# Kernel tuning notes

Hardware: AMD Instinct MI355X
Metric: run time of the kernel (lower is better)

## Reference

```python
import jax, jax.numpy as jnp
import numpy as np
from jax.ops import segment_sum, segment_max

N_NODES, N_EDGES, N_GRAPHS = 50000, 800000, 128
IN_C, HID, HEADS, CLIN = 64, 64, 4, 32


def gat_layer(x, W, a_s, a_d, b, src, dst, n):
    # GAT-style attention conv with concatenated heads (PyG GATConv math).
    H, C = a_s.shape
    h = (x @ W).reshape(-1, H, C)                      # [N,H,C]
    es = jnp.einsum('nhc,hc->nh', h, a_s)
    ed = jnp.einsum('nhc,hc->nh', h, a_d)
    e = jax.nn.leaky_relu(es[src] + ed[dst], 0.2)      # [E,H]
    m = segment_max(e, dst, num_segments=n)            # stable softmax over incoming edges
    e = jnp.exp(e - m[dst])
    denom = segment_sum(e, dst, num_segments=n)
    alpha = e / jnp.where(denom[dst] > 0, denom[dst], 1.0)
    out = segment_sum(h[src] * alpha[:, :, None], dst, num_segments=n)  # [N,H,C]
    return out.reshape(-1, H * C) + b


def label_prop(x, src, dst, n, num_layers=2, alpha=0.5):
    # PyG LabelPropagation: sym-normalized diffusion, residual mix, clamp to [0,1].
    deg = segment_sum(jnp.ones((src.shape[0],), x.dtype), dst, num_segments=n)
    dis = jnp.where(deg > 0, 1.0 / jnp.sqrt(jnp.maximum(deg, 1.0)), 0.0)
    norm = (dis[src] * dis[dst])[:, None]
    res = (1.0 - alpha) * x
    out = x
    for _ in range(num_layers):
        out = alpha * segment_sum(out[src] * norm, dst, num_segments=n) + res
        out = jnp.clip(out, 0.0, 1.0)
    return out


def mean_pool(x, batch, n_graphs):
    cnt = segment_sum(jnp.ones((x.shape[0],), x.dtype), batch, num_segments=n_graphs)
    s = segment_sum(x, batch, num_segments=n_graphs)
    return s / jnp.maximum(cnt, 1.0)[:, None]


def setup_inputs() -> dict:
    key = jax.random.key(0)
    ks = iter(jax.random.split(key, 32))
    def p(shape, fan_in):
        return jax.random.normal(next(ks), shape, jnp.float32) / np.sqrt(fan_in)
    d = {}
    d['x'] = jax.random.normal(next(ks), (N_NODES, IN_C), jnp.float32)
    d['edge_index'] = jax.random.randint(next(ks), (2, N_EDGES), 0, N_NODES)
    d['batch'] = jnp.sort(jax.random.randint(next(ks), (N_NODES,), 0, N_GRAPHS))
    d['clinical_data'] = jax.random.normal(next(ks), (N_GRAPHS, CLIN), jnp.float32)
    HC = HEADS * HID
    d['W1'] = p((IN_C, HC), IN_C); d['a1s'] = p((HEADS, HID), HID); d['a1d'] = p((HEADS, HID), HID); d['b1'] = jnp.zeros((HC,), jnp.float32)
    d['W2'] = p((HC, HC), HC); d['a2s'] = p((HEADS, HID), HID); d['a2d'] = p((HEADS, HID), HID); d['b2'] = jnp.zeros((HC,), jnp.float32)
    jk = IN_C + 2 * HC  # 576
    d['pp_w1'] = p((jk, 256), jk); d['pp_b1'] = jnp.zeros((256,), jnp.float32)
    d['pp_w2'] = p((256, 128), 256); d['pp_b2'] = jnp.zeros((128,), jnp.float32)
    d['cl_w1'] = p((CLIN, 64), CLIN); d['cl_b1'] = jnp.zeros((64,), jnp.float32)
    d['cl_w2'] = p((64, 32), 64); d['cl_b2'] = jnp.zeros((32,), jnp.float32)
    d['h_w1'] = p((160, 64), 160); d['h_b1'] = jnp.zeros((64,), jnp.float32)
    d['h_w2'] = p((64, 32), 64); d['h_b2'] = jnp.zeros((32,), jnp.float32)
    d['h_w3'] = p((32, 2), 32); d['h_b3'] = jnp.zeros((2,), jnp.float32)
    return d


def reference(x, edge_index, batch, clinical_data,
              W1, a1s, a1d, b1, W2, a2s, a2d, b2,
              pp_w1, pp_b1, pp_w2, pp_b2,
              cl_w1, cl_b1, cl_w2, cl_b2,
              h_w1, h_b1, h_w2, h_b2, h_w3, h_b3):
    src, dst = edge_index[0], edge_index[1]
    n = x.shape[0]
    h0 = x
    h1 = jax.nn.relu(gat_layer(h0, W1, a1s, a1d, b1, src, dst, n))
    h1 = label_prop(h1, src, dst, n)
    h2 = jax.nn.relu(gat_layer(h1, W2, a2s, a2d, b2, src, dst, n))
    h2 = label_prop(h2, src, dst, n)
    combined = jnp.concatenate([h0, h1, h2], axis=-1)           # [N, 576]
    g = mean_pool(combined, batch, N_GRAPHS)                    # [G, 576]
    v_graph = jax.nn.relu(g @ pp_w1 + pp_b1) @ pp_w2 + pp_b2    # [G, 128] (dropout = eval/no-op)
    v_clin = jax.nn.relu(clinical_data @ cl_w1 + cl_b1) @ cl_w2 + cl_b2  # [G, 32]
    z = jnp.concatenate([v_graph, v_clin], axis=-1)             # [G, 160]
    z = jax.nn.relu(z @ h_w1 + h_b1)
    z = jax.nn.relu(z @ h_w2 + h_b2)
    return z @ h_w3 + h_b3                                      # [G, 2]
```

## Files before the change

### kernel.cpp

```cpp
#include <hip/hip_runtime.h>

#define N_NODES 50000
#define N_EDGES 800000
#define N_GRAPHS 128
#define JK 576
#define CAP 192
#define NSB ((N_NODES + 255) / 256)

typedef __attribute__((ext_vector_type(8))) short bf16x8;
typedef __attribute__((ext_vector_type(4))) float f32x4;

__device__ __forceinline__ unsigned f2_to_bf2(float a, float b) {
    unsigned ua = __float_as_uint(a), ub = __float_as_uint(b);
    ua = (ua + 0x7fffu + ((ua >> 16) & 1u)) >> 16;
    ub = (ub + 0x7fffu + ((ub >> 16) & 1u)) >> 16;
    return ua | (ub << 16);
}
__device__ __forceinline__ uint2 f4_to_bf4(float4 v) {
    return make_uint2(f2_to_bf2(v.x, v.y), f2_to_bf2(v.z, v.w));
}
__device__ __forceinline__ float4 bf4_to_f4(uint2 u) {
    float4 r;
    r.x = __uint_as_float(u.x << 16);
    r.y = __uint_as_float(u.x & 0xffff0000u);
    r.z = __uint_as_float(u.y << 16);
    r.w = __uint_as_float(u.y & 0xffff0000u);
    return r;
}

template<int BN, int KK>
__global__ __launch_bounds__(256)
void mfma_gemm(const unsigned short* __restrict__ Abf, int lda,
               const unsigned short* __restrict__ BT,
               unsigned* __restrict__ Cbf, int ldc,
               int M, const float* __restrict__ bias, int relu,
               int a_off, int b_off, int c_off) {
    __shared__ unsigned short As[64][32];
    __shared__ unsigned short Bs[BN][32];
    const int t = threadIdx.x;
    const int wav = t >> 6, lane = t & 63;
    const int quad = lane >> 4, l15 = lane & 15;
    const int m0 = blockIdx.x * 64;
    const int head = blockIdx.y;
    Abf += (size_t)head * a_off;
    BT  += (size_t)head * b_off;
    const float* bptr = bias ? bias + (size_t)head * c_off : nullptr;
    unsigned* cbf = Cbf + (((size_t)head * c_off) >> 1);

    f32x4 acc[BN / 16];
#pragma unroll
    for (int i = 0; i < BN / 16; i++) acc[i] = (f32x4){0.f, 0.f, 0.f, 0.f};

    const int arow = t >> 2, aseg = t & 3;
    for (int k0 = 0; k0 < KK; k0 += 32) {
        uint4 av = make_uint4(0, 0, 0, 0);
        int gm = m0 + arow;
        if (gm < M) av = *(const uint4*)&Abf[(size_t)gm * lda + k0 + aseg * 8];
        uint4 bv[BN == 256 ? 4 : 1];
        if (BN == 256) {
            const unsigned short* srcb = &BT[(size_t)t * KK + k0];
#pragma unroll
            for (int j = 0; j < 4; j++) bv[j] = *(const uint4*)&srcb[j * 8];
        } else {
            bv[0] = *(const uint4*)&BT[(size_t)arow * KK + k0 + aseg * 8];
        }
        __syncthreads();
        *(uint4*)&As[arow][aseg * 8] = av;
        if (BN == 256) {
#pragma unroll
            for (int j = 0; j < 4; j++) *(uint4*)&Bs[t][j * 8] = bv[j];
        } else {
            *(uint4*)&Bs[arow][aseg * 8] = bv[0];
        }
        __syncthreads();
        bf16x8 afrag = *(const bf16x8*)&As[wav * 16 + l15][quad * 8];
#pragma unroll
        for (int nt = 0; nt < BN / 16; nt++) {
            bf16x8 bfrag = *(const bf16x8*)&Bs[nt * 16 + l15][quad * 8];
            acc[nt] = __builtin_amdgcn_mfma_f32_16x16x32_bf16(afrag, bfrag, acc[nt], 0, 0, 0);
        }
    }
    int rbase = m0 + wav * 16 + quad * 4;
#pragma unroll
    for (int nt = 0; nt < BN / 16; nt++) {
        int col = nt * 16 + l15;
        float bb = bptr ? bptr[col] : 0.f;
#pragma unroll
        for (int r = 0; r < 4; r++) {
            int row = rbase + r;
            float v = acc[nt][r] + bb;
            if (relu) v = fmaxf(v, 0.f);
            float vp = __shfl_xor(v, 1);
            if (row < M && !(l15 & 1))
                cbf[((size_t)row * ldc + col) >> 1] = f2_to_bf2(v, vp);
        }
    }
}

__global__ void deg_kernel(const int* __restrict__ dst, int* __restrict__ deg,
                           const int* __restrict__ batch, int* __restrict__ gstart) {
    int t = blockIdx.x * blockDim.x + threadIdx.x;
    if (t < N_EDGES) {
        atomicAdd(&deg[dst[t]], 1);
    } else if (t < N_EDGES + N_NODES) {
        int n = t - N_EDGES;
        int b = batch[n];
        int prev = (n == 0) ? -1 : batch[n - 1];
        for (int g = prev + 1; g <= b; g++) gstart[g] = n;
        if (n == N_NODES - 1)
            for (int g = b + 1; g <= N_GRAPHS; g++) gstart[g] = N_NODES;
    }
}

#define S1 50000
#define S2 50256
#define S3 51280
#define S4 67664
#define S5 133200
#define S6 1733200
#define S7 (S6 + 131072)
__global__ void prep_misc(const int* __restrict__ deg, float* __restrict__ dis,
                          const float* __restrict__ W1, const float* __restrict__ a1s,
                          const float* __restrict__ a1d, float* __restrict__ wes1,
                          float* __restrict__ wed1,
                          const float* __restrict__ W2, const float* __restrict__ a2s,
                          const float* __restrict__ a2d, float* __restrict__ wes2,
                          float* __restrict__ wed2,
                          unsigned short* __restrict__ W1T, unsigned short* __restrict__ W2T,
                          const float* __restrict__ x, unsigned* __restrict__ xbf,
                          const int* __restrict__ gstart, float* __restrict__ psum) {
    int i = blockIdx.x * blockDim.x + threadIdx.x;
    if (i >= S7) return;
    if (i >= S6) {
        int t2 = i - S6;
        int g = t2 >> 10, rem = t2 & 1023;
        int q = rem >> 8, tid = rem & 255;
        int cp = tid & 63, np = tid >> 6;
        int n0 = gstart[g], n1 = gstart[g + 1];
        int len = n1 - n0;
        int ns = n0 + (len * q) / 4, ne = n0 + (len * (q + 1)) / 4;
        float s = 0.f;
        for (int n = ns + np; n < ne; n += 4) s += x[(size_t)n * 64 + cp];
        atomicAdd(&psum[g * JK + cp], s);
    } else if (i >= S5) {
        int j = i - S5;
        float2 v = *(const float2*)&x[(size_t)j * 2];
        xbf[j] = f2_to_bf2(v.x, v.y);
    } else if (i >= S4) {
        int t2 = i - S4;
        int n = t2 >> 8, c = t2 & 255;
        unsigned u = __float_as_uint(W2[(size_t)c * 256 + n]);
        u = (u + 0x7fffu + ((u >> 16) & 1u)) >> 16;
        W2T[t2] = (unsigned short)u;
    } else if (i >= S3) {
        int t2 = i - S3;
        int n = t2 >> 6, c = t2 & 63;
        unsigned u = __float_as_uint(W1[(size_t)c * 256 + n]);
        u = (u + 0x7fffu + ((u >> 16) & 1u)) >> 16;
        W1T[t2] = (unsigned short)u;
    } else if (i >= S2) {
        int t2 = i - S2;
        int c = t2 >> 2, h = t2 & 3;
        float se = 0.f, sd = 0.f;
        for (int j = 0; j < 64; j++) {
            float w = W2[(size_t)c * 256 + h * 64 + j];
            se += w * a2s[h * 64 + j];
            sd += w * a2d[h * 64 + j];
        }
        wes2[c * 4 + h] = se;
        wed2[c * 4 + h] = sd;
    } else if (i >= S1) {
        int t2 = i - S1;
        int c = t2 >> 2, h = t2 & 3;
        float se = 0.f, sd = 0.f;
        for (int j = 0; j < 64; j++) {
            float w = W1[(size_t)c * 256 + h * 64 + j];
            se += w * a1s[h * 64 + j];
            sd += w * a1d[h * 64 + j];
        }
        wes1[c * 4 + h] = se;
        wed1[c * 4 + h] = sd;
    } else {
        int d = deg[i];
        dis[i] = d > 0 ? rsqrtf((float)d) : 0.f;
    }
}
__global__ __launch_bounds__(256) void scan_bsum(const int* __restrict__ deg,
                                                 int* __restrict__ bsum) {
    __shared__ int sd[256];
    int n = blockIdx.x * 256 + threadIdx.x;
    sd[threadIdx.x] = (n < N_NODES) ? deg[n] : 0;
    __syncthreads();
    for (int o = 128; o > 0; o >>= 1) {
        if (threadIdx.x < o) sd[threadIdx.x] += sd[threadIdx.x + o];
        __syncthreads();
    }
    if (threadIdx.x == 0) bsum[blockIdx.x] = sd[0];
}
__global__ __launch_bounds__(256) void scan_bpre(const int* __restrict__ bsum,
                                                 int* __restrict__ bpre,
                                                 int* __restrict__ off_last) {
    __shared__ int sd[256];
    int t = threadIdx.x;
    int v = (t < NSB) ? bsum[t] : 0;
    sd[t] = v;
    __syncthreads();
    for (int o = 1; o < 256; o <<= 1) {
        int u = (t >= o) ? sd[t - o] : 0;
        __syncthreads();
        sd[t] += u;
        __syncthreads();
    }
    if (t < NSB) bpre[t] = sd[t] - v;
    if (t == 255) *off_last = sd[255];
}
__global__ __launch_bounds__(256) void scan_off(const int* __restrict__ deg,
                                                const int* __restrict__ bpre,
                                                int* __restrict__ off) {
    __shared__ int sd[256];
    int n = blockIdx.x * 256 + threadIdx.x;
    int t = threadIdx.x;
    int v = (n < N_NODES) ? deg[n] : 0;
    sd[t] = v;
    __syncthreads();
    for (int o = 1; o < 256; o <<= 1) {
        int u = (t >= o) ? sd[t - o] : 0;
        __syncthreads();
        sd[t] += u;
        __syncthreads();
    }
    if (n < N_NODES) off[n] = bpre[blockIdx.x] + sd[t] - v;
}
__global__ void csr_fill(const int* __restrict__ src, const int* __restrict__ dst,
                         const int* __restrict__ off, int* __restrict__ cursor,
                         int* __restrict__ csr_src) {
    int e = blockIdx.x * blockDim.x + threadIdx.x;
    if (e >= N_EDGES) return;
    int s = src[e], d = dst[e];
    int pos = off[d] + atomicAdd(&cursor[d], 1);
    csr_src[pos] = s;
}

__global__ void esed_x(const float* __restrict__ X, const float* __restrict__ wes,
                       const float* __restrict__ wed, float* __restrict__ es,
                       float* __restrict__ ed) {
    int gid = blockIdx.x * blockDim.x + threadIdx.x;
    int n = gid >> 6, lane = threadIdx.x & 63;
    if (n >= N_NODES) return;
    float xv = X[(size_t)n * 64 + lane];
    float4 a = *(const float4*)&wes[lane * 4];
    float4 b = *(const float4*)&wed[lane * 4];
    float4 ps = make_float4(xv * a.x, xv * a.y, xv * a.z, xv * a.w);
    float4 pd = make_float4(xv * b.x, xv * b.y, xv * b.z, xv * b.w);
#pragma unroll
    for (int o = 1; o < 64; o <<= 1) {
        ps.x += __shfl_xor(ps.x, o); ps.y += __shfl_xor(ps.y, o);
        ps.z += __shfl_xor(ps.z, o); ps.w += __shfl_xor(ps.w, o);
        pd.x += __shfl_xor(pd.x, o); pd.y += __shfl_xor(pd.y, o);
        pd.z += __shfl_xor(pd.z, o); pd.w += __shfl_xor(pd.w, o);
    }
    if (lane == 0) {
        *(float4*)&es[n * 4] = ps;
        *(float4*)&ed[n * 4] = pd;
    }
}

__global__ __launch_bounds__(256)
void gat1_fused(const int* __restrict__ off, const int* __restrict__ csr_src,
                const float* __restrict__ es, const float* __restrict__ ed,
                const unsigned* __restrict__ xbf, unsigned* __restrict__ aggx_bf,
                float* __restrict__ alpha_fb) {
    __shared__ float elds[4][CAP * 4];
    __shared__ int   sidx[4][CAP];
    int wav = threadIdx.x >> 6, lane = threadIdx.x & 63;
    int n = blockIdx.x * 4 + wav;
    bool active = n < N_NODES;
    int p0 = 0, p1 = 0;
    float4 ed4 = make_float4(0.f, 0.f, 0.f, 0.f);
    if (active) { p0 = off[n]; p1 = off[n + 1]; ed4 = *(const float4*)&ed[n * 4]; }
    float4 sum = make_float4(0.f, 0.f, 0.f, 0.f);
    for (int p = p0 + lane; p < p1; p += 64) {
        int s = csr_src[p];
        float4 e4 = *(const float4*)&es[s * 4];
        e4.x += ed4.x; e4.y += ed4.y; e4.z += ed4.z; e4.w += ed4.w;
        e4.x = e4.x > 0.f ? e4.x : 0.2f * e4.x;
        e4.y = e4.y > 0.f ? e4.y : 0.2f * e4.y;
        e4.z = e4.z > 0.f ? e4.z : 0.2f * e4.z;
        e4.w = e4.w > 0.f ? e4.w : 0.2f * e4.w;
        e4.x = __expf(e4.x); e4.y = __expf(e4.y); e4.z = __expf(e4.z); e4.w = __expf(e4.w);
        int q = p - p0;
        if (q < CAP) { *(float4*)&elds[wav][q * 4] = e4; sidx[wav][q] = s; }
        else         *(float4*)&alpha_fb[(size_t)p * 4] = e4;
        sum.x += e4.x; sum.y += e4.y; sum.z += e4.z; sum.w += e4.w;
    }
#pragma unroll
    for (int o = 1; o < 64; o <<= 1) {
        sum.x += __shfl_xor(sum.x, o); sum.y += __shfl_xor(sum.y, o);
        sum.z += __shfl_xor(sum.z, o); sum.w += __shfl_xor(sum.w, o);
    }
    float4 rs;
    rs.x = sum.x > 0.f ? 1.f / sum.x : 0.f;
    rs.y = sum.y > 0.f ? 1.f / sum.y : 0.f;
    rs.z = sum.z > 0.f ? 1.f / sum.z : 0.f;
    rs.w = sum.w > 0.f ? 1.f / sum.w : 0.f;
    if (!active) return;
    int eg = lane >> 4, l15 = lane & 15;
    int deg = p1 - p0;
    float4 a0 = make_float4(0.f, 0.f, 0.f, 0.f);
    float4 a1 = a0, a2 = a0, a3 = a0;
    auto fetch = [&](int qq, float4& e4, float4& xv) {
        e4 = make_float4(0.f, 0.f, 0.f, 0.f);
        xv = e4;
        if (qq < deg) {
            int s;
            if (qq < CAP) { s = sidx[wav][qq]; e4 = *(const float4*)&elds[wav][qq * 4]; }
            else { s = csr_src[p0 + qq]; e4 = *(const float4*)&alpha_fb[(size_t)(p0 + qq) * 4]; }
            xv = bf4_to_f4(*(const uint2*)&xbf[(size_t)s * 32 + l15 * 2]);
        }
    };
    int q = eg;
    float4 eA, xA, eB, xB, eC, xC;
    fetch(q, eA, xA);
    fetch(q + 4, eB, xB);
    fetch(q + 8, eC, xC);
    while (q < deg) {
        float4 eD, xD;
        fetch(q + 12, eD, xD);
        a0.x += eA.x * xA.x; a0.y += eA.x * xA.y; a0.z += eA.x * xA.z; a0.w += eA.x * xA.w;
        a1.x += eA.y * xA.x; a1.y += eA.y * xA.y; a1.z += eA.y * xA.z; a1.w += eA.y * xA.w;
        a2.x += eA.z * xA.x; a2.y += eA.z * xA.y; a2.z += eA.z * xA.z; a2.w += eA.z * xA.w;
        a3.x += eA.w * xA.x; a3.y += eA.w * xA.y; a3.z += eA.w * xA.z; a3.w += eA.w * xA.w;
        eA = eB; xA = xB; eB = eC; xB = xC; eC = eD; xC = xD;
        q += 4;
    }
#pragma unroll
    for (int o = 16; o < 64; o <<= 1) {
        a0.x += __shfl_xor(a0.x, o); a0.y += __shfl_xor(a0.y, o);
        a0.z += __shfl_xor(a0.z, o); a0.w += __shfl_xor(a0.w, o);
        a1.x += __shfl_xor(a1.x, o); a1.y += __shfl_xor(a1.y, o);
        a1.z += __shfl_xor(a1.z, o); a1.w += __shfl_xor(a1.w, o);
        a2.x += __shfl_xor(a2.x, o); a2.y += __shfl_xor(a2.y, o);
        a2.z += __shfl_xor(a2.z, o); a2.w += __shfl_xor(a2.w, o);
        a3.x += __shfl_xor(a3.x, o); a3.y += __shfl_xor(a3.y, o);
        a3.z += __shfl_xor(a3.z, o); a3.w += __shfl_xor(a3.w, o);
    }
    if (eg == 0) {
        a0.x *= rs.x; a0.y *= rs.x; a0.z *= rs.x; a0.w *= rs.x;
        a1.x *= rs.y; a1.y *= rs.y; a1.z *= rs.y; a1.w *= rs.y;
        a2.x *= rs.z; a2.y *= rs.z; a2.z *= rs.z; a2.w *= rs.z;
        a3.x *= rs.w; a3.y *= rs.w; a3.z *= rs.w; a3.w *= rs.w;
        size_t b = (size_t)n * 128 + l15 * 2;
        *(uint2*)&aggx_bf[b +  0] = f4_to_bf4(a0);
        *(uint2*)&aggx_bf[b + 32] = f4_to_bf4(a1);
        *(uint2*)&aggx_bf[b + 64] = f4_to_bf4(a2);
        *(uint2*)&aggx_bf[b + 96] = f4_to_bf4(a3);
    }
}

__global__ __launch_bounds__(256)
void gat2_fused(const int* __restrict__ off, const int* __restrict__ csr_src,
                const float* __restrict__ es, const float* __restrict__ ed,
                const unsigned* __restrict__ H2bf, const float* __restrict__ bias,
                unsigned* __restrict__ outbf, float* __restrict__ alpha_fb) {
    __shared__ float elds[4][CAP * 4];
    __shared__ int   sidx[4][CAP];
    int wav = threadIdx.x >> 6, lane = threadIdx.x & 63;
    int n = blockIdx.x * 4 + wav;
    bool active = n < N_NODES;
    int p0 = 0, p1 = 0;
    float4 ed4 = make_float4(0.f, 0.f, 0.f, 0.f);
    if (active) { p0 = off[n]; p1 = off[n + 1]; ed4 = *(const float4*)&ed[n * 4]; }
    float4 sum = make_float4(0.f, 0.f, 0.f, 0.f);
    for (int p = p0 + lane; p < p1; p += 64) {
        int s = csr_src[p];
        float4 e4 = *(const float4*)&es[s * 4];
        e4.x += ed4.x; e4.y += ed4.y; e4.z += ed4.z; e4.w += ed4.w;
        e4.x = e4.x > 0.f ? e4.x : 0.2f * e4.x;
        e4.y = e4.y > 0.f ? e4.y : 0.2f * e4.y;
        e4.z = e4.z > 0.f ? e4.z : 0.2f * e4.z;
        e4.w = e4.w > 0.f ? e4.w : 0.2f * e4.w;
        e4.x = __expf(e4.x); e4.y = __expf(e4.y); e4.z = __expf(e4.z); e4.w = __expf(e4.w);
        int q = p - p0;
        if (q < CAP) { *(float4*)&elds[wav][q * 4] = e4; sidx[wav][q] = s; }
        else         *(float4*)&alpha_fb[(size_t)p * 4] = e4;
        sum.x += e4.x; sum.y += e4.y; sum.z += e4.z; sum.w += e4.w;
    }
#pragma unroll
    for (int o = 1; o < 64; o <<= 1) {
        sum.x += __shfl_xor(sum.x, o); sum.y += __shfl_xor(sum.y, o);
        sum.z += __shfl_xor(sum.z, o); sum.w += __shfl_xor(sum.w, o);
    }
    if (!active) return;
    int half = lane >> 5, l = lane & 31;
    int hh = l >> 3;
    float sh = (hh == 0) ? sum.x : (hh == 1) ? sum.y : (hh == 2) ? sum.z : sum.w;
    float rsh = sh > 0.f ? 1.f / sh : 0.f;
    int deg = p1 - p0;
    float acc[8];
#pragma unroll
    for (int j = 0; j < 8; j++) acc[j] = 0.f;
    auto fetch = [&](int qq, float& al, uint4& rr) {
        al = 0.f;
        rr = make_uint4(0, 0, 0, 0);
        if (qq < deg) {
            int s;
            if (qq < CAP) { s = sidx[wav][qq]; al = elds[wav][qq * 4 + hh]; }
            else { s = csr_src[p0 + qq]; al = alpha_fb[(size_t)(p0 + qq) * 4 + hh]; }
            rr = *(const uint4*)&H2bf[(size_t)s * 128 + l * 4];
        }
    };
    int q = half;
    float aA, aB, aC;
    uint4 rA, rB, rC;
    fetch(q, aA, rA);
    fetch(q + 2, aB, rB);
    fetch(q + 4, aC, rC);
    while (q < deg) {
        float aD; uint4 rD;
        fetch(q + 6, aD, rD);
        float4 f0 = bf4_to_f4(make_uint2(rA.x, rA.y));
        float4 f1 = bf4_to_f4(make_uint2(rA.z, rA.w));
        acc[0] += aA * f0.x; acc[1] += aA * f0.y; acc[2] += aA * f0.z; acc[3] += aA * f0.w;
        acc[4] += aA * f1.x; acc[5] += aA * f1.y; acc[6] += aA * f1.z; acc[7] += aA * f1.w;
        aA = aB; rA = rB; aB = aC; rB = rC; aC = aD; rC = rD;
        q += 2;
    }
#pragma unroll
    for (int j = 0; j < 8; j++) acc[j] += __shfl_xor(acc[j], 32);
    if (half == 0) {
        float4 b0 = *(const float4*)&bias[l * 8];
        float4 b1 = *(const float4*)&bias[l * 8 + 4];
        float4 o0, o1;
        o0.x = fmaxf(acc[0] * rsh + b0.x, 0.f);
        o0.y = fmaxf(acc[1] * rsh + b0.y, 0.f);
        o0.z = fmaxf(acc[2] * rsh + b0.z, 0.f);
        o0.w = fmaxf(acc[3] * rsh + b0.w, 0.f);
        o1.x = fmaxf(acc[4] * rsh + b1.x, 0.f);
        o1.y = fmaxf(acc[5] * rsh + b1.y, 0.f);
        o1.z = fmaxf(acc[6] * rsh + b1.z, 0.f);
        o1.w = fmaxf(acc[7] * rsh + b1.w, 0.f);
        uint2 w0 = f4_to_bf4(o0), w1 = f4_to_bf4(o1);
        uint4 w = make_uint4(w0.x, w0.y, w1.x, w1.y);
        *(uint4*)&outbf[(size_t)n * 128 + l * 4] = w;
    }
}

template<int FUSE_ESED>
__global__ __launch_bounds__(256)
void lp_csr_t(const int* __restrict__ off, const int* __restrict__ csr_src,
              const float* __restrict__ dis, const unsigned* __restrict__ in_bf,
              const unsigned* __restrict__ res_bf, unsigned* __restrict__ out_bf,
              const float* __restrict__ wes, const float* __restrict__ wed,
              float* __restrict__ es, float* __restrict__ ed) {
    __shared__ int   widx[4][CAP];
    __shared__ float wwt[4][CAP];
    int wav = threadIdx.x >> 6, lane = threadIdx.x & 63;
    int n = blockIdx.x * 4 + wav;
    if (n >= N_NODES) return;
    int p0 = off[n], p1 = off[n + 1];
    int deg = p1 - p0;
    float disd = dis[n];
    for (int q = lane; q < deg && q < CAP; q += 64) {
        int s = csr_src[p0 + q];
        widx[wav][q] = s;
        wwt[wav][q] = dis[s] * disd;
    }
    int half = lane >> 5, l = lane & 31;
    float acc[8];
#pragma unroll
    for (int j = 0; j < 8; j++) acc[j] = 0.f;
    auto fetch = [&](int qq, float& nw, uint4& rr) {
        nw = 0.f;
        rr = make_uint4(0, 0, 0, 0);
        if (qq < deg) {
            int s;
            if (qq < CAP) { s = widx[wav][qq]; nw = wwt[wav][qq]; }
            else { s = csr_src[p0 + qq]; nw = dis[s] * disd; }
            rr = *(const uint4*)&in_bf[(size_t)s * 128 + l * 4];
        }
    };
    int q = half;
    float nA, nB, nC;
    uint4 rA, rB, rC;
    fetch(q, nA, rA);
    fetch(q + 2, nB, rB);
    fetch(q + 4, nC, rC);
    while (q < deg) {
        float nD; uint4 rD;
        fetch(q + 6, nD, rD);
        float4 f0 = bf4_to_f4(make_uint2(rA.x, rA.y));
        float4 f1 = bf4_to_f4(make_uint2(rA.z, rA.w));
        acc[0] += nA * f0.x; acc[1] += nA * f0.y; acc[2] += nA * f0.z; acc[3] += nA * f0.w;
        acc[4] += nA * f1.x; acc[5] += nA * f1.y; acc[6] += nA * f1.z; acc[7] += nA * f1.w;
        nA = nB; rA = rB; nB = nC; rB = rC; nC = nD; rC = rD;
        q += 2;
    }
#pragma unroll
    for (int j = 0; j < 8; j++) acc[j] += __shfl_xor(acc[j], 32);
    if (half == 0) {
        uint4 rr = *(const uint4*)&res_bf[(size_t)n * 128 + l * 4];
        float4 r0 = bf4_to_f4(make_uint2(rr.x, rr.y));
        float4 r1 = bf4_to_f4(make_uint2(rr.z, rr.w));
        float4 o0, o1;
        o0.x = fminf(fmaxf(0.5f * acc[0] + 0.5f * r0.x, 0.f), 1.f);
        o0.y = fminf(fmaxf(0.5f * acc[1] + 0.5f * r0.y, 0.f), 1.f);
        o0.z = fminf(fmaxf(0.5f * acc[2] + 0.5f * r0.z, 0.f), 1.f);
        o0.w = fminf(fmaxf(0.5f * acc[3] + 0.5f * r0.w, 0.f), 1.f);
        o1.x = fminf(fmaxf(0.5f * acc[4] + 0.5f * r1.x, 0.f), 1.f);
        o1.y = fminf(fmaxf(0.5f * acc[5] + 0.5f * r1.y, 0.f), 1.f);
        o1.z = fminf(fmaxf(0.5f * acc[6] + 0.5f * r1.z, 0.f), 1.f);
        o1.w = fminf(fmaxf(0.5f * acc[7] + 0.5f * r1.w, 0.f), 1.f);
        uint2 w0 = f4_to_bf4(o0), w1 = f4_to_bf4(o1);
        uint4 w = make_uint4(w0.x, w0.y, w1.x, w1.y);
        *(uint4*)&out_bf[(size_t)n * 128 + l * 4] = w;
        if (FUSE_ESED) {
            float vv[8] = {o0.x, o0.y, o0.z, o0.w, o1.x, o1.y, o1.z, o1.w};
            float4 ps = make_float4(0.f, 0.f, 0.f, 0.f);
            float4 pd = make_float4(0.f, 0.f, 0.f, 0.f);
#pragma unroll
            for (int j = 0; j < 8; j++) {
                int c = l * 8 + j;
                float4 a = *(const float4*)&wes[c * 4];
                float4 b = *(const float4*)&wed[c * 4];
                ps.x += vv[j] * a.x; ps.y += vv[j] * a.y; ps.z += vv[j] * a.z; ps.w += vv[j] * a.w;
                pd.x += vv[j] * b.x; pd.y += vv[j] * b.y; pd.z += vv[j] * b.z; pd.w += vv[j] * b.w;
            }
#pragma unroll
            for (int o = 1; o < 32; o <<= 1) {
                ps.x += __shfl_xor(ps.x, o); ps.y += __shfl_xor(ps.y, o);
                ps.z += __shfl_xor(ps.z, o); ps.w += __shfl_xor(ps.w, o);
                pd.x += __shfl_xor(pd.x, o); pd.y += __shfl_xor(pd.y, o);
                pd.z += __shfl_xor(pd.z, o); pd.w += __shfl_xor(pd.w, o);
            }
            if (l == 0) {
                *(float4*)&es[n * 4] = ps;
                *(float4*)&ed[n * 4] = pd;
            }
        }
    }
}

__global__ void pool_bf(const unsigned* __restrict__ buf, const int* __restrict__ gstart,
                        float* __restrict__ psum, int colOff) {
    int g = blockIdx.x, q = blockIdx.y;
    int n0 = gstart[g], n1 = gstart[g + 1];
    int len = n1 - n0;
    int ns = n0 + (len * q) / 4, ne = n0 + (len * (q + 1)) / 4;
    int cp = threadIdx.x & 127;
    int np = threadIdx.x >> 7;
    float s0 = 0.f, s1 = 0.f;
    for (int n = ns + np; n < ne; n += 2) {
        unsigned u = buf[(size_t)n * 128 + cp];
        s0 += __uint_as_float(u << 16);
        s1 += __uint_as_float(u & 0xffff0000u);
    }
    atomicAdd(&psum[g * JK + colOff + cp * 2 + 0], s0);
    atomicAdd(&psum[g * JK + colOff + cp * 2 + 1], s1);
}

__global__ __launch_bounds__(256)
void head_all(const float* __restrict__ psum, const int* __restrict__ gstart,
              const float* __restrict__ clin,
              const float* __restrict__ pp_w1, const float* __restrict__ pp_b1,
              const float* __restrict__ pp_w2, const float* __restrict__ pp_b2,
              const float* __restrict__ cl_w1, const float* __restrict__ cl_b1,
              const float* __restrict__ cl_w2, const float* __restrict__ cl_b2,
              const float* __restrict__ h_w1, const float* __restrict__ h_b1,
              const float* __restrict__ h_w2, const float* __restrict__ h_b2,
              const float* __restrict__ h_w3, const float* __restrict__ h_b3,
              float* __restrict__ out) {
    __shared__ float zin[JK];
    __shared__ float z1[256];
    __shared__ float zcl[32];
    __shared__ float zc[64];
    __shared__ float z[160];
    __shared__ float z3[64];
    __shared__ float z4[32];
    __shared__ float part[128];
    int g = blockIdx.x, t = threadIdx.x;
    int len = gstart[g + 1] - gstart[g];
    float inv = 1.f / (float)(len > 1 ? len : 1);
    for (int k = t; k < JK; k += 256) zin[k] = psum[g * JK + k] * inv;
    if (t < 32) zcl[t] = clin[g * 32 + t];
    __syncthreads();
    {
        float acc = pp_b1[t];
#pragma unroll 8
        for (int k = 0; k < JK; k++) acc += zin[k] * pp_w1[k * 256 + t];
        z1[t] = fmaxf(acc, 0.f);
    }
    __syncthreads();
    int m = t & 127, half = t >> 7;
    {
        float acc = 0.f;
        int k0 = half * 128;
#pragma unroll 8
        for (int k = k0; k < k0 + 128; k++) acc += z1[k] * pp_w2[k * 128 + m];
        if (half) part[m] = acc;
        __syncthreads();
        if (!half) z[m] = acc + part[m] + pp_b2[m];
    }
    if (t < 64) {
        float acc = cl_b1[t];
#pragma unroll
        for (int k = 0; k < 32; k++) acc += zcl[k] * cl_w1[k * 64 + t];
        zc[t] = fmaxf(acc, 0.f);
    }
    __syncthreads();
    if (t < 32) {
        float acc = cl_b2[t];
#pragma unroll
        for (int k = 0; k < 64; k++) acc += zc[k] * cl_w2[k * 32 + t];
        z[128 + t] = acc;
    }
    __syncthreads();
    if (t < 64) {
        float acc = h_b1[t];
#pragma unroll 8
        for (int k = 0; k < 160; k++) acc += z[k] * h_w1[k * 64 + t];
        z3[t] = fmaxf(acc, 0.f);
    }
    __syncthreads();
    if (t < 32) {
        float acc = h_b2[t];
#pragma unroll
        for (int k = 0; k < 64; k++) acc += z3[k] * h_w2[k * 32 + t];
        z4[t] = fmaxf(acc, 0.f);
    }
    __syncthreads();
    if (t < 2) {
        float acc = h_b3[t];
#pragma unroll
        for (int k = 0; k < 32; k++) acc += z4[k] * h_w3[k * 2 + t];
        out[g * 2 + t] = acc;
    }
}

extern "C" void kernel_launch(void* const* d_in, const int* in_sizes, int n_in,
                              void* d_out, int out_size, void* d_ws, size_t ws_size,
                              hipStream_t stream) {
    const float* x     = (const float*)d_in[0];
    const int*   ei    = (const int*)d_in[1];
    const int*   batch = (const int*)d_in[2];
    const float* clin  = (const float*)d_in[3];
    const float* W1  = (const float*)d_in[4];
    const float* a1s = (const float*)d_in[5];
    const float* a1d = (const float*)d_in[6];
    const float* b1  = (const float*)d_in[7];
    const float* W2  = (const float*)d_in[8];
    const float* a2s = (const float*)d_in[9];
    const float* a2d = (const float*)d_in[10];
    const float* b2  = (const float*)d_in[11];
    const float* pp_w1 = (const float*)d_in[12];
    const float* pp_b1 = (const float*)d_in[13];
    const float* pp_w2 = (const float*)d_in[14];
    const float* pp_b2 = (const float*)d_in[15];
    const float* cl_w1 = (const float*)d_in[16];
    const float* cl_b1 = (const float*)d_in[17];
    const float* cl_w2 = (const float*)d_in[18];
    const float* cl_b2 = (const float*)d_in[19];
    const float* h_w1  = (const float*)d_in[20];
    const float* h_b1  = (const float*)d_in[21];
    const float* h_w2  = (const float*)d_in[22];
    const float* h_b2  = (const float*)d_in[23];
    const float* h_w3  = (const float*)d_in[24];
    const float* h_b3  = (const float*)d_in[25];

    const int* src = ei;
    const int* dst = ei + N_EDGES;

    char* p = (char*)d_ws;
    auto carve = [&](size_t bytes) -> char* {
        char* r = p;
        p += (bytes + 255) & ~(size_t)255;
        return r;
    };
    const size_t NBH = (size_t)N_NODES * 256 * 2;
    unsigned* abf  = (unsigned*)carve(NBH);
    unsigned* bf1  = (unsigned*)carve(NBH);
    unsigned* bf2  = (unsigned*)carve(NBH);
    unsigned* bf3  = (unsigned*)carve(NBH);
    unsigned* xbf  = (unsigned*)carve((size_t)N_NODES * 32 * 4);
    float* alpha_fb  = (float*)carve((size_t)N_EDGES * 4 * 4);
    int*   csr_src   = (int*)carve((size_t)N_EDGES * 4);
    int*   off       = (int*)carve((size_t)(N_NODES + 1) * 4);
    int*   deg       = (int*)carve((size_t)N_NODES * 4);
    int*   cursor    = (int*)carve((size_t)N_NODES * 4);
    int*   bsum      = (int*)carve((size_t)NSB * 4);
    int*   bpre      = (int*)carve((size_t)NSB * 4);
    float* dis       = (float*)carve((size_t)N_NODES * 4);
    float* es        = (float*)carve((size_t)N_NODES * 4 * 4);
    float* ed        = (float*)carve((size_t)N_NODES * 4 * 4);
    float* wes1      = (float*)carve((size_t)64 * 4 * 4);
    float* wed1      = (float*)carve((size_t)64 * 4 * 4);
    float* wes2      = (float*)carve((size_t)256 * 4 * 4);
    float* wed2      = (float*)carve((size_t)256 * 4 * 4);
    unsigned short* W1T = (unsigned short*)carve((size_t)256 * 64 * 2);
    unsigned short* W2T = (unsigned short*)carve((size_t)256 * 256 * 2);
    int*   gstart    = (int*)carve((size_t)(N_GRAPHS + 1) * 4);
    float* psum      = (float*)carve((size_t)N_GRAPHS * JK * 4);

    const int TB = 256;
    const int gE     = (N_EDGES + TB - 1) / TB;
    const int gDeg   = (N_EDGES + N_NODES + TB - 1) / TB;
    const int gNwave = (N_NODES * 64 + TB - 1) / TB;
    const int gFuse  = (N_NODES + 3) / 4;
    const int gRow   = (N_NODES + 63) / 64;
    const int gPrep  = (S7 + TB - 1) / TB;

    hipMemsetAsync(deg, 0, (size_t)N_NODES * 4, stream);
    hipMemsetAsync(cursor, 0, (size_t)N_NODES * 4, stream);
    hipMemsetAsync(psum, 0, (size_t)N_GRAPHS * JK * 4, stream);
    deg_kernel<<<gDeg, TB, 0, stream>>>(dst, deg, batch, gstart);
    prep_misc<<<gPrep, TB, 0, stream>>>(deg, dis,
                                        W1, a1s, a1d, wes1, wed1,
                                        W2, a2s, a2d, wes2, wed2,
                                        W1T, W2T, x, xbf, gstart, psum);
    scan_bsum<<<NSB, 256, 0, stream>>>(deg, bsum);
    scan_bpre<<<1, 256, 0, stream>>>(bsum, bpre, &off[N_NODES]);
    scan_off<<<NSB, 256, 0, stream>>>(deg, bpre, off);
    csr_fill<<<gE, TB, 0, stream>>>(src, dst, off, cursor, csr_src);

    esed_x<<<gNwave, TB, 0, stream>>>(x, wes1, wed1, es, ed);
    gat1_fused<<<gFuse, TB, 0, stream>>>(off, csr_src, es, ed, xbf, abf, alpha_fb);
    mfma_gemm<64, 64><<<dim3(gRow, 4), 256, 0, stream>>>(
        (const unsigned short*)abf, 256, W1T, bf1, 256, N_NODES, b1, 1,
        64, 64 * 64, 64);

    lp_csr_t<0><<<gFuse, TB, 0, stream>>>(off, csr_src, dis, bf1, bf1, bf2,
                                          nullptr, nullptr, nullptr, nullptr);
    lp_csr_t<1><<<gFuse, TB, 0, stream>>>(off, csr_src, dis, bf2, bf1, bf3,
                                          wes2, wed2, es, ed);

    pool_bf<<<dim3(N_GRAPHS, 4), TB, 0, stream>>>(bf3, gstart, psum, 64);

    mfma_gemm<256, 256><<<dim3(gRow, 1), 256, 0, stream>>>(
        (const unsigned short*)bf3, 256, W2T, bf1, 256, N_NODES, nullptr, 0,
        0, 0, 0);
    gat2_fused<<<gFuse, TB, 0, stream>>>(off, csr_src, es, ed, bf1, b2, bf2, alpha_fb);

    lp_csr_t<0><<<gFuse, TB, 0, stream>>>(off, csr_src, dis, bf2, bf2, bf1,
                                          nullptr, nullptr, nullptr, nullptr);
    lp_csr_t<0><<<gFuse, TB, 0, stream>>>(off, csr_src, dis, bf1, bf2, abf,
                                          nullptr, nullptr, nullptr, nullptr);

    pool_bf<<<dim3(N_GRAPHS, 4), TB, 0, stream>>>(abf, gstart, psum, 320);
    head_all<<<N_GRAPHS, 256, 0, stream>>>(psum, gstart, clin,
                                           pp_w1, pp_b1, pp_w2, pp_b2,
                                           cl_w1, cl_b1, cl_w2, cl_b2,
                                           h_w1, h_b1, h_w2, h_b2, h_w3, h_b3,
                                           (float*)d_out);
}
```

Measured before the change: 767.1 us.

## Stage label-prop neighbor gathers through LDS with async global_load_lds double buffering

Rewrites the label-propagation CSR gather so neighbor feature rows are loaded with global_load_lds straight into a per-wave double-buffered LDS region, four edges per batch. Explicit vmcnt waits overlap the next batch's loads with accumulation of the current one, replacing the register-rotated prefetch. Edge lists are padded to multiples of four with zero-weight entries pointing at node 0. This adds 16KB of LDS per block, which may lower occupancy, and depends on the LDS write layout of the load-to-LDS builtin being correct.

New measurement: 770.1 us. Within noise of the previous version (+0.4%).

```diff
diff --git a/kernel.cpp b/kernel.cpp
--- a/kernel.cpp
+++ b/kernel.cpp
@@ -27,6 +27,11 @@
     r.w = __uint_as_float(u.y & 0xffff0000u);
     return r;
 }
+
+__device__ __forceinline__ void gll16(const unsigned* g, unsigned* l) {
+    __builtin_amdgcn_global_load_lds(g, l, 16, 0, 0);
+}
+#define WAITVM(N) asm volatile("s_waitcnt vmcnt(" #N ")" ::: "memory")
 
 template<int BN, int KK>
 __global__ __launch_bounds__(256)
@@ -452,48 +457,73 @@
               const unsigned* __restrict__ res_bf, unsigned* __restrict__ out_bf,
               const float* __restrict__ wes, const float* __restrict__ wed,
               float* __restrict__ es, float* __restrict__ ed) {
-    __shared__ int   widx[4][CAP];
-    __shared__ float wwt[4][CAP];
+    __shared__ int      widx[4][CAP];
+    __shared__ float    wwt[4][CAP];
+    __shared__ unsigned sedge[4][2][512];
     int wav = threadIdx.x >> 6, lane = threadIdx.x & 63;
     int n = blockIdx.x * 4 + wav;
     if (n >= N_NODES) return;
     int p0 = off[n], p1 = off[n + 1];
     int deg = p1 - p0;
     float disd = dis[n];
-    for (int q = lane; q < deg && q < CAP; q += 64) {
-        int s = csr_src[p0 + q];
+    int dmain = deg < CAP ? deg : CAP;
+    int padded = (dmain + 3) & ~3;
+    for (int q = lane; q < padded; q += 64) {
+        int s = 0; float w = 0.f;
+        if (q < dmain) { s = csr_src[p0 + q]; w = dis[s] * disd; }
         widx[wav][q] = s;
-        wwt[wav][q] = dis[s] * disd;
+        wwt[wav][q]  = w;
     }
     int half = lane >> 5, l = lane & 31;
     float acc[8];
 #pragma unroll
     for (int j = 0; j < 8; j++) acc[j] = 0.f;
-    auto fetch = [&](int qq, float& nw, uint4& rr) {
-        nw = 0.f;
-        rr = make_uint4(0, 0, 0, 0);
-        if (qq < deg) {
-            int s;
-            if (qq < CAP) { s = widx[wav][qq]; nw = wwt[wav][qq]; }
-            else { s = csr_src[p0 + qq]; nw = dis[s] * disd; }
-            rr = *(const uint4*)&in_bf[(size_t)s * 128 + l * 4];
+
+    int nb = padded >> 2;
+    auto issue = [&](int b) {
+        int base = b * 4;
+        int bsel = b & 1;
+#pragma unroll
+        for (int jj = 0; jj < 2; jj++) {
+            int s = widx[wav][base + 2 * jj + half];
+            gll16(&in_bf[(size_t)s * 128 + l * 4], &sedge[wav][bsel][jj * 256]);
         }
     };
-    int q = half;
-    float nA, nB, nC;
-    uint4 rA, rB, rC;
-    fetch(q, nA, rA);
-    fetch(q + 2, nB, rB);
-    fetch(q + 4, nC, rC);
-    while (q < deg) {
-        float nD; uint4 rD;
-        fetch(q + 6, nD, rD);
-        float4 f0 = bf4_to_f4(make_uint2(rA.x, rA.y));
-        float4 f1 = bf4_to_f4(make_uint2(rA.z, rA.w));
-        acc[0] += nA * f0.x; acc[1] += nA * f0.y; acc[2] += nA * f0.z; acc[3] += nA * f0.w;
-        acc[4] += nA * f1.x; acc[5] += nA * f1.y; acc[6] += nA * f1.z; acc[7] += nA * f1.w;
-        nA = nB; rA = rB; nB = nC; rB = rC; nC = nD; rC = rD;
-        q += 2;
+    if (nb > 0) {
+        issue(0);
+        for (int b = 0; b < nb; b++) {
+            if (b + 1 < nb) {
+                issue(b + 1);
+                WAITVM(2);
+            } else {
+                WAITVM(0);
+            }
+            __builtin_amdgcn_sched_barrier(0);
+            int base = b * 4, bsel = b & 1;
+#pragma unroll
+            for (int j = 0; j < 2; j++) {
+                int e = 2 * j + half;
+                uint4 rr = *(const uint4*)&sedge[wav][bsel][e * 128 + l * 4];
+                float nw = wwt[wav][base + e];
+                float4 f0 = bf4_to_f4(make_uint2(rr.x, rr.y));
+                float4 f1 = bf4_to_f4(make_uint2(rr.z, rr.w));
+                acc[0] += nw * f0.x; acc[1] += nw * f0.y;
+                acc[2] += nw * f0.z; acc[3] += nw * f0.w;
+                acc[4] += nw * f1.x; acc[5] += nw * f1.y;
+                acc[6] += nw * f1.z; acc[7] += nw * f1.w;
+            }
+        }
+    }
+    for (int q = CAP + half; q < deg; q += 2) {
+        int s = csr_src[p0 + q];
+        float nw = dis[s] * disd;
+        uint4 rr = *(const uint4*)&in_bf[(size_t)s * 128 + l * 4];
+        float4 f0 = bf4_to_f4(make_uint2(rr.x, rr.y));
+        float4 f1 = bf4_to_f4(make_uint2(rr.z, rr.w));
+        acc[0] += nw * f0.x; acc[1] += nw * f0.y;
+        acc[2] += nw * f0.z; acc[3] += nw * f0.w;
+        acc[4] += nw * f1.x; acc[5] += nw * f1.y;
+        acc[6] += nw * f1.z; acc[7] += nw * f1.w;
     }
 #pragma unroll
     for (int j = 0; j < 8; j++) acc[j] += __shfl_xor(acc[j], 32);
```

## Store hidden features in 32-channel slices and split label propagation per slice

Applied to the files above, without the earlier changes.

Hidden activations move from row-major [N,256] bf16 to eight channel-slice planes of 32 channels each. The GEMMs, pooling and GAT2 output are updated to read and write this layout. Label propagation now runs one wave per node per slice, so each gather touches a compact 64-byte row that fits cache better. The attention-score computation that was fused into label propagation becomes a separate esed_h kernel. In exchange, CSR indices and dis values are re-read once per slice (8x more), and there is an extra kernel launch.

Measured after the change: 1.126 ms. 1.47x slower.

```diff
diff --git a/kernel.cpp b/kernel.cpp
--- a/kernel.cpp
+++ b/kernel.cpp
@@ -6,6 +6,7 @@
 #define JK 576
 #define CAP 192
 #define NSB ((N_NODES + 255) / 256)
+#define SLICE_U (N_NODES * 16)
 
 typedef __attribute__((ext_vector_type(8))) short bf16x8;
 typedef __attribute__((ext_vector_type(4))) float f32x4;
@@ -28,7 +29,7 @@
     return r;
 }
 
-template<int BN, int KK>
+template<int BN, int KK, int SLA, int SLC>
 __global__ __launch_bounds__(256)
 void mfma_gemm(const unsigned short* __restrict__ Abf, int lda,
                const unsigned short* __restrict__ BT,
@@ -42,7 +43,7 @@
     const int quad = lane >> 4, l15 = lane & 15;
     const int m0 = blockIdx.x * 64;
     const int head = blockIdx.y;
-    Abf += (size_t)head * a_off;
+    const unsigned short* Ab = Abf + (size_t)head * a_off;
     BT  += (size_t)head * b_off;
     const float* bptr = bias ? bias + (size_t)head * c_off : nullptr;
     unsigned* cbf = Cbf + (((size_t)head * c_off) >> 1);
@@ -55,7 +56,14 @@
     for (int k0 = 0; k0 < KK; k0 += 32) {
         uint4 av = make_uint4(0, 0, 0, 0);
         int gm = m0 + arow;
-        if (gm < M) av = *(const uint4*)&Abf[(size_t)gm * lda + k0 + aseg * 8];
+        if (gm < M) {
+            if (SLA) {
+                av = *(const uint4*)&Ab[(size_t)(k0 >> 5) * (N_NODES * 32) +
+                                        (size_t)gm * 32 + aseg * 8];
+            } else {
+                av = *(const uint4*)&Ab[(size_t)gm * lda + k0 + aseg * 8];
+            }
+        }
         uint4 bv[BN == 256 ? 4 : 1];
         if (BN == 256) {
             const unsigned short* srcb = &BT[(size_t)t * KK + k0];
@@ -91,8 +99,15 @@
             float v = acc[nt][r] + bb;
             if (relu) v = fmaxf(v, 0.f);
             float vp = __shfl_xor(v, 1);
-            if (row < M && !(l15 & 1))
-                cbf[((size_t)row * ldc + col) >> 1] = f2_to_bf2(v, vp);
+            if (row < M && !(l15 & 1)) {
+                if (SLC) {
+                    int ch = head * c_off + col;
+                    size_t a = (size_t)(ch >> 5) * SLICE_U + (size_t)row * 16 + ((ch & 31) >> 1);
+                    Cbf[a] = f2_to_bf2(v, vp);
+                } else {
+                    cbf[((size_t)row * ldc + col) >> 1] = f2_to_bf2(v, vp);
+                }
+            }
         }
     }
 }
@@ -265,6 +280,47 @@
     }
 }
 
+__global__ void esed_h(const unsigned* __restrict__ Hsl, const float* __restrict__ wes,
+                       const float* __restrict__ wed, float* __restrict__ es,
+                       float* __restrict__ ed) {
+    int gid = blockIdx.x * blockDim.x + threadIdx.x;
+    int n = gid >> 6, lane = threadIdx.x & 63;
+    if (n >= N_NODES) return;
+    int sl = lane >> 3;
+    uint2 u = *(const uint2*)&Hsl[(size_t)sl * SLICE_U + (size_t)n * 16 + (lane & 7) * 2];
+    float4 vv = bf4_to_f4(u);
+    float v0 = vv.x, v1 = vv.y, v2 = vv.z, v3 = vv.w;
+    int ch0 = lane * 4;
+    float4 a0 = *(const float4*)&wes[(ch0 + 0) * 4];
+    float4 a1 = *(const float4*)&wes[(ch0 + 1) * 4];
+    float4 a2 = *(const float4*)&wes[(ch0 + 2) * 4];
+    float4 a3 = *(const float4*)&wes[(ch0 + 3) * 4];
+    float4 b0 = *(const float4*)&wed[(ch0 + 0) * 4];
+    float4 b1 = *(const float4*)&wed[(ch0 + 1) * 4];
+    float4 b2 = *(const float4*)&wed[(ch0 + 2) * 4];
+    float4 b3 = *(const float4*)&wed[(ch0 + 3) * 4];
+    float4 ps, pd;
+    ps.x = v0 * a0.x + v1 * a1.x + v2 * a2.x + v3 * a3.x;
+    ps.y = v0 * a0.y + v1 * a1.y + v2 * a2.y + v3 * a3.y;
+    ps.z = v0 * a0.z + v1 * a1.z + v2 * a2.z + v3 * a3.z;
+    ps.w = v0 * a0.w + v1 * a1.w + v2 * a2.w + v3 * a3.w;
+    pd.x = v0 * b0.x + v1 * b1.x + v2 * b2.x + v3 * b3.x;
+    pd.y = v0 * b0.y + v1 * b1.y + v2 * b2.y + v3 * b3.y;
+    pd.z = v0 * b0.z + v1 * b1.z + v2 * b2.z + v3 * b3.z;
+    pd.w = v0 * b0.w + v1 * b1.w + v2 * b2.w + v3 * b3.w;
+#pragma unroll
+    for (int o = 1; o < 64; o <<= 1) {
+        ps.x += __shfl_xor(ps.x, o); ps.y += __shfl_xor(ps.y, o);
+        ps.z += __shfl_xor(ps.z, o); ps.w += __shfl_xor(ps.w, o);
+        pd.x += __shfl_xor(pd.x, o); pd.y += __shfl_xor(pd.y, o);
+        pd.z += __shfl_xor(pd.z, o); pd.w += __shfl_xor(pd.w, o);
+    }
+    if (lane == 0) {
+        *(float4*)&es[n * 4] = ps;
+        *(float4*)&ed[n * 4] = pd;
+    }
+}
+
 __global__ __launch_bounds__(256)
 void gat1_fused(const int* __restrict__ off, const int* __restrict__ csr_src,
                 const float* __restrict__ es, const float* __restrict__ ed,
@@ -441,64 +497,45 @@
         o1.w = fmaxf(acc[7] * rsh + b1.w, 0.f);
         uint2 w0 = f4_to_bf4(o0), w1 = f4_to_bf4(o1);
         uint4 w = make_uint4(w0.x, w0.y, w1.x, w1.y);
-        *(uint4*)&outbf[(size_t)n * 128 + l * 4] = w;
-    }
-}
-
-template<int FUSE_ESED>
+        size_t a = (size_t)(l >> 2) * SLICE_U + (size_t)n * 16 + (l & 3) * 4;
+        *(uint4*)&outbf[a] = w;
+    }
+}
+
 __global__ __launch_bounds__(256)
-void lp_csr_t(const int* __restrict__ off, const int* __restrict__ csr_src,
-              const float* __restrict__ dis, const unsigned* __restrict__ in_bf,
-              const unsigned* __restrict__ res_bf, unsigned* __restrict__ out_bf,
-              const float* __restrict__ wes, const float* __restrict__ wed,
-              float* __restrict__ es, float* __restrict__ ed) {
-    __shared__ int   widx[4][CAP];
-    __shared__ float wwt[4][CAP];
+void lp_slice(const int* __restrict__ off, const int* __restrict__ csr_src,
+              const float* __restrict__ dis, const unsigned* __restrict__ in_sl,
+              const unsigned* __restrict__ res_sl, unsigned* __restrict__ out_sl) {
     int wav = threadIdx.x >> 6, lane = threadIdx.x & 63;
-    int n = blockIdx.x * 4 + wav;
+    int sl = blockIdx.x & 7, chunk = blockIdx.x >> 3;
+    int n = chunk * 4 + wav;
     if (n >= N_NODES) return;
     int p0 = off[n], p1 = off[n + 1];
-    int deg = p1 - p0;
     float disd = dis[n];
-    for (int q = lane; q < deg && q < CAP; q += 64) {
-        int s = csr_src[p0 + q];
-        widx[wav][q] = s;
-        wwt[wav][q] = dis[s] * disd;
-    }
-    int half = lane >> 5, l = lane & 31;
+    int e4 = lane >> 2, seg = lane & 3;
+    const unsigned* base = in_sl + (size_t)sl * SLICE_U;
     float acc[8];
 #pragma unroll
     for (int j = 0; j < 8; j++) acc[j] = 0.f;
-    auto fetch = [&](int qq, float& nw, uint4& rr) {
-        nw = 0.f;
-        rr = make_uint4(0, 0, 0, 0);
-        if (qq < deg) {
-            int s;
-            if (qq < CAP) { s = widx[wav][qq]; nw = wwt[wav][qq]; }
-            else { s = csr_src[p0 + qq]; nw = dis[s] * disd; }
-            rr = *(const uint4*)&in_bf[(size_t)s * 128 + l * 4];
-        }
-    };
-    int q = half;
-    float nA, nB, nC;
-    uint4 rA, rB, rC;
-    fetch(q, nA, rA);
-    fetch(q + 2, nB, rB);
-    fetch(q + 4, nC, rC);
-    while (q < deg) {
-        float nD; uint4 rD;
-        fetch(q + 6, nD, rD);
-        float4 f0 = bf4_to_f4(make_uint2(rA.x, rA.y));
-        float4 f1 = bf4_to_f4(make_uint2(rA.z, rA.w));
-        acc[0] += nA * f0.x; acc[1] += nA * f0.y; acc[2] += nA * f0.z; acc[3] += nA * f0.w;
-        acc[4] += nA * f1.x; acc[5] += nA * f1.y; acc[6] += nA * f1.z; acc[7] += nA * f1.w;
-        nA = nB; rA = rB; nB = nC; rB = rC; nC = nD; rC = rD;
-        q += 2;
-    }
-#pragma unroll
-    for (int j = 0; j < 8; j++) acc[j] += __shfl_xor(acc[j], 32);
-    if (half == 0) {
-        uint4 rr = *(const uint4*)&res_bf[(size_t)n * 128 + l * 4];
+    for (int p = p0 + e4; p < p1; p += 16) {
+        int s = csr_src[p];
+        float nw = dis[s] * disd;
+        uint4 rr = *(const uint4*)&base[(size_t)s * 16 + seg * 4];
+        float4 f0 = bf4_to_f4(make_uint2(rr.x, rr.y));
+        float4 f1 = bf4_to_f4(make_uint2(rr.z, rr.w));
+        acc[0] += nw * f0.x; acc[1] += nw * f0.y;
+        acc[2] += nw * f0.z; acc[3] += nw * f0.w;
+        acc[4] += nw * f1.x; acc[5] += nw * f1.y;
+        acc[6] += nw * f1.z; acc[7] += nw * f1.w;
+    }
+#pragma unroll
+    for (int o = 4; o < 64; o <<= 1) {
+#pragma unroll
+        for (int j = 0; j < 8; j++) acc[j] += __shfl_xor(acc[j], o);
+    }
+    if (e4 == 0) {
+        size_t a = (size_t)sl * SLICE_U + (size_t)n * 16 + seg * 4;
+        uint4 rr = *(const uint4*)&res_sl[a];
         float4 r0 = bf4_to_f4(make_uint2(rr.x, rr.y));
         float4 r1 = bf4_to_f4(make_uint2(rr.z, rr.w));
         float4 o0, o1;
@@ -511,32 +548,7 @@
         o1.z = fminf(fmaxf(0.5f * acc[6] + 0.5f * r1.z, 0.f), 1.f);
         o1.w = fminf(fmaxf(0.5f * acc[7] + 0.5f * r1.w, 0.f), 1.f);
         uint2 w0 = f4_to_bf4(o0), w1 = f4_to_bf4(o1);
-        uint4 w = make_uint4(w0.x, w0.y, w1.x, w1.y);
-        *(uint4*)&out_bf[(size_t)n * 128 + l * 4] = w;
-        if (FUSE_ESED) {
-            float vv[8] = {o0.x, o0.y, o0.z, o0.w, o1.x, o1.y, o1.z, o1.w};
-            float4 ps = make_float4(0.f, 0.f, 0.f, 0.f);
-            float4 pd = make_float4(0.f, 0.f, 0.f, 0.f);
-#pragma unroll
-            for (int j = 0; j < 8; j++) {
-                int c = l * 8 + j;
-                float4 a = *(const float4*)&wes[c * 4];
-                float4 b = *(const float4*)&wed[c * 4];
-                ps.x += vv[j] * a.x; ps.y += vv[j] * a.y; ps.z += vv[j] * a.z; ps.w += vv[j] * a.w;
-                pd.x += vv[j] * b.x; pd.y += vv[j] * b.y; pd.z += vv[j] * b.z; pd.w += vv[j] * b.w;
-            }
-#pragma unroll
-            for (int o = 1; o < 32; o <<= 1) {
-                ps.x += __shfl_xor(ps.x, o); ps.y += __shfl_xor(ps.y, o);
-                ps.z += __shfl_xor(ps.z, o); ps.w += __shfl_xor(ps.w, o);
-                pd.x += __shfl_xor(pd.x, o); pd.y += __shfl_xor(pd.y, o);
-                pd.z += __shfl_xor(pd.z, o); pd.w += __shfl_xor(pd.w, o);
-            }
-            if (l == 0) {
-                *(float4*)&es[n * 4] = ps;
-                *(float4*)&ed[n * 4] = pd;
-            }
-        }
+        *(uint4*)&out_sl[a] = make_uint4(w0.x, w0.y, w1.x, w1.y);
     }
 }
 
@@ -548,9 +560,10 @@
     int ns = n0 + (len * q) / 4, ne = n0 + (len * (q + 1)) / 4;
     int cp = threadIdx.x & 127;
     int np = threadIdx.x >> 7;
+    size_t sbase = (size_t)(cp >> 4) * SLICE_U + (cp & 15);
     float s0 = 0.f, s1 = 0.f;
     for (int n = ns + np; n < ne; n += 2) {
-        unsigned u = buf[(size_t)n * 128 + cp];
+        unsigned u = buf[sbase + (size_t)n * 16];
         s0 += __uint_as_float(u << 16);
         s1 += __uint_as_float(u & 0xffff0000u);
     }
@@ -707,6 +720,7 @@
     const int gFuse  = (N_NODES + 3) / 4;
     const int gRow   = (N_NODES + 63) / 64;
     const int gPrep  = (S7 + TB - 1) / TB;
+    const int gSlice = 8 * ((N_NODES + 3) / 4);
 
     hipMemsetAsync(deg, 0, (size_t)N_NODES * 4, stream);
     hipMemsetAsync(cursor, 0, (size_t)N_NODES * 4, stream);
@@ -723,26 +737,23 @@
 
     esed_x<<<gNwave, TB, 0, stream>>>(x, wes1, wed1, es, ed);
     gat1_fused<<<gFuse, TB, 0, stream>>>(off, csr_src, es, ed, xbf, abf, alpha_fb);
-    mfma_gemm<64, 64><<<dim3(gRow, 4), 256, 0, stream>>>(
+    mfma_gemm<64, 64, 0, 1><<<dim3(gRow, 4), 256, 0, stream>>>(
         (const unsigned short*)abf, 256, W1T, bf1, 256, N_NODES, b1, 1,
         64, 64 * 64, 64);
 
-    lp_csr_t<0><<<gFuse, TB, 0, stream>>>(off, csr_src, dis, bf1, bf1, bf2,
-                                          nullptr, nullptr, nullptr, nullptr);
-    lp_csr_t<1><<<gFuse, TB, 0, stream>>>(off, csr_src, dis, bf2, bf1, bf3,
-                                          wes2, wed2, es, ed);
+    lp_slice<<<gSlice, TB, 0, stream>>>(off, csr_src, dis, bf1, bf1, bf2);
+    lp_slice<<<gSlice, TB, 0, stream>>>(off, csr_src, dis, bf2, bf1, bf3);
+    esed_h<<<gNwave, TB, 0, stream>>>(bf3, wes2, wed2, es, ed);
 
     pool_bf<<<dim3(N_GRAPHS, 4), TB, 0, stream>>>(bf3, gstart, psum, 64);
 
-    mfma_gemm<256, 256><<<dim3(gRow, 1), 256, 0, stream>>>(
+    mfma_gemm<256, 256, 1, 0><<<dim3(gRow, 1), 256, 0, stream>>>(
         (const unsigned short*)bf3, 256, W2T, bf1, 256, N_NODES, nullptr, 0,
         0, 0, 0);
     gat2_fused<<<gFuse, TB, 0, stream>>>(off, csr_src, es, ed, bf1, b2, bf2, alpha_fb);
 
-    lp_csr_t<0><<<gFuse, TB, 0, stream>>>(off, csr_src, dis, bf2, bf2, bf1,
-                                          nullptr, nullptr, nullptr, nullptr);
-    lp_csr_t<0><<<gFuse, TB, 0, stream>>>(off, csr_src, dis, bf1, bf2, abf,
-                                          nullptr, nullptr, nullptr, nullptr);
+    lp_slice<<<gSlice, TB, 0, stream>>>(off, csr_src, dis, bf2, bf2, bf1);
+    lp_slice<<<gSlice, TB, 0, stream>>>(off, csr_src, dis, bf1, bf2, abf);
 
     pool_bf<<<dim3(N_GRAPHS, 4), TB, 0, stream>>>(abf, gstart, psum, 320);
     head_all<<<N_GRAPHS, 256, 0, stream>>>(psum, gstart, clin,
```
